# Optimization experiments

Measured on AMD Instinct MI355X. Metric: run time of the kernel, lower is better.

The kernel has to match this reference:

```python
import jax, jax.numpy as jnp
import numpy as np

B, N, E = 2, 20000, 160000
D, U = 1, 100          # input_dim, num_units
IN = D + U             # 101
NEG_SLOPE = 0.2        # PyG GATv2Conv default


def setup_inputs() -> dict:
    key = jax.random.key(0)
    ks = jax.random.split(key, 20)
    s = 0.1
    inp = {
        "inputs": jax.random.normal(ks[0], (B, N * D), jnp.float32),
        "state": jax.random.normal(ks[1], (B, N * U), jnp.float32),
        "src": jax.random.randint(ks[2], (E,), 0, N),
        "dst": jax.random.randint(ks[3], (E,), 0, N),
        # GATv2Conv(101, 200) params: lin_l, lin_r, att, out-bias
        "Wl1": jax.random.normal(ks[4], (IN, 2 * U), jnp.float32) * s,
        "bl1": jax.random.normal(ks[5], (2 * U,), jnp.float32) * s,
        "Wr1": jax.random.normal(ks[6], (IN, 2 * U), jnp.float32) * s,
        "br1": jax.random.normal(ks[7], (2 * U,), jnp.float32) * s,
        "att1": jax.random.normal(ks[8], (2 * U,), jnp.float32) * s,
        "bg1": jax.random.normal(ks[9], (2 * U,), jnp.float32) * s,
        "bias0": jax.random.normal(ks[10], (2 * U,), jnp.float32) * s,
        # GATv2Conv(101, 100) params
        "Wl2": jax.random.normal(ks[11], (IN, U), jnp.float32) * s,
        "bl2": jax.random.normal(ks[12], (U,), jnp.float32) * s,
        "Wr2": jax.random.normal(ks[13], (IN, U), jnp.float32) * s,
        "br2": jax.random.normal(ks[14], (U,), jnp.float32) * s,
        "att2": jax.random.normal(ks[15], (U,), jnp.float32) * s,
        "bg2": jax.random.normal(ks[16], (U,), jnp.float32) * s,
        "bias1": jax.random.normal(ks[17], (U,), jnp.float32) * s,
    }
    return inp


def _gatv2(x, src_f, dst_f, Wl, bl, Wr, br, att, bg):
    # x: (B, N, IN); edges (with self-loops) flow src -> dst.
    xl = x @ Wl + bl                                   # (B, N, C) source transform
    xr = x @ Wr + br                                   # (B, N, C) target transform
    msg = jax.nn.leaky_relu(xl[:, src_f] + xr[:, dst_f], NEG_SLOPE)  # (B, Ef, C)
    e = jnp.einsum('bec,c->be', msg, att)              # (B, Ef) attention logits
    seg_max = jax.vmap(lambda v: jax.ops.segment_max(v, dst_f, num_segments=N))(e)
    ea = jnp.exp(e - seg_max[:, dst_f])
    denom = jax.vmap(lambda v: jax.ops.segment_sum(v, dst_f, num_segments=N))(ea)
    alpha = ea / denom[:, dst_f]                       # per-target softmax
    out = jax.vmap(
        lambda a, xs: jax.ops.segment_sum(a[:, None] * xs, dst_f, num_segments=N)
    )(alpha, xl[:, src_f])                             # (B, N, C)
    return out + bg


def reference(inputs, state, src, dst,
              Wl1, bl1, Wr1, br1, att1, bg1, bias0,
              Wl2, bl2, Wr2, br2, att2, bg2, bias1):
    loops = jnp.arange(N)
    src_f = jnp.concatenate([src, loops])              # PyG adds self-loops
    dst_f = jnp.concatenate([dst, loops])
    inputs3 = inputs.reshape(B, N, D)
    state3 = state.reshape(B, N, U)

    # _gc1: GATv2(101 -> 200) + bias_0, sigmoid gates r, u
    xs = jnp.concatenate([inputs3, state3], axis=2)    # (B, N, 101)
    g1 = _gatv2(xs, src_f, dst_f, Wl1, bl1, Wr1, br1, att1, bg1) + bias0
    val = jax.nn.sigmoid(g1)                           # (B, N, 200)
    r = val[..., :U].reshape(B, N * U)
    u = val[..., U:].reshape(B, N * U)

    # _gc2: GATv2(101 -> 100) on [inputs, r*state] + bias_1, tanh
    xs2 = jnp.concatenate([inputs3, (r * state).reshape(B, N, U)], axis=2)
    c = jnp.tanh(_gatv2(xs2, src_f, dst_f, Wl2, bl2, Wr2, br2, att2, bg2) + bias1)
    c = c.reshape(B, N * U)

    new_state = u * state + (1.0 - u) * c              # (B, N*U)
    return new_state
```

## Files before the change

### kernel.cpp

```cpp
#include <hip/hip_runtime.h>
#include <stdint.h>

typedef __attribute__((ext_vector_type(8))) short short8;
typedef __attribute__((ext_vector_type(4))) short short4v;
typedef __attribute__((ext_vector_type(4))) float f32x4;

static constexpr int BB = 2, NN = 20000, UU = 100;
static constexpr int MT = BB * NN;
static constexpr int MPAD = 40192;
static constexpr float NEG = 0.2f;

__device__ __forceinline__ float b2f(short s) {
  union { uint32_t u; float f; } cv; cv.u = ((uint32_t)(uint16_t)s) << 16; return cv.f;
}
__device__ __forceinline__ short f2b(float x) {
  union { float f; uint32_t u; } cv; cv.f = x;
  uint32_t r = cv.u + 0x7FFFu + ((cv.u >> 16) & 1u);
  return (short)(r >> 16);
}

template<int CTRL>
__device__ __forceinline__ float dppadd(float x) {
  int v = __builtin_amdgcn_update_dpp(0, __float_as_int(x), CTRL, 0xF, 0xF, false);
  return x + __int_as_float(v);
}
__device__ __forceinline__ float red32(float x) {
  x = dppadd<0x121>(x);
  x = dppadd<0x122>(x);
  x = dppadd<0x124>(x);
  x = dppadd<0x128>(x);
  return x + __shfl_xor(x, 16);
}


__global__ void k_prep(const float* __restrict__ inp, const float* __restrict__ st,
                       const float* __restrict__ Wl1, const float* __restrict__ Wr1,
                       const float* __restrict__ Wl2, const float* __restrict__ Wr2,
                       short* __restrict__ A, short* __restrict__ BT1,
                       short* __restrict__ BT2, int* __restrict__ cursor) {
  int t = blockIdx.x * 256 + threadIdx.x;
  if (t < MT * 16) {
    int r = t >> 4, g = t & 15;
    short8 v;
#pragma unroll
    for (int j = 0; j < 8; ++j) {
      int e = g * 8 + j;
      float x = 0.f;
      if (e == 0) x = inp[r];
      else if (e <= 100) x = st[(size_t)r * 100 + e - 1];
      v[j] = f2b(x);
    }
    *(short8*)(A + (size_t)r * 128 + (g << 3)) = v;
  }
  if (t < 512 * 16) {
    int n = t >> 4, g = t & 15;
    short8 v;
#pragma unroll
    for (int j = 0; j < 8; ++j) {
      int k = g * 8 + j;
      float x = 0.f;
      if (k < 101 && n < 400)
        x = (n < 200) ? Wl1[(size_t)k * 200 + n] : Wr1[(size_t)k * 200 + n - 200];
      v[j] = f2b(x);
    }
    *(short8*)(BT1 + (size_t)n * 128 + (g << 3)) = v;
  }
  if (t < 256 * 16) {
    int n = t >> 4, g = t & 15;
    short8 v;
#pragma unroll
    for (int j = 0; j < 8; ++j) {
      int k = g * 8 + j;
      int ksrc = (k < 100) ? k + 1 : ((k == 100) ? 0 : -1);
      float x = 0.f;
      if (ksrc >= 0 && n < 200)
        x = (n < 100) ? Wl2[(size_t)ksrc * 100 + n] : Wr2[(size_t)ksrc * 100 + n - 100];
      v[j] = f2b(x);
    }
    *(short8*)(BT2 + (size_t)n * 128 + (g << 3)) = v;
  }
  if (t < NN) cursor[t] = 0;
}


__global__ void k_hist(const int* __restrict__ dst, int E, int* __restrict__ hist) {
  int e = blockIdx.x * 256 + threadIdx.x;
  if (e < E) atomicAdd(&hist[dst[e]], 1);
}

__global__ __launch_bounds__(1024) void k_scan(int* __restrict__ histcur,
                                               int* __restrict__ rowptr, int N, int E) {
  __shared__ int part[1024];
  int t = threadIdx.x;
  int CH = (N + 1023) / 1024;
  int beg = t * CH; if (beg > N) beg = N;
  int end = beg + CH; if (end > N) end = N;
  int s = 0;
  for (int i = beg; i < end; ++i) s += histcur[i];
  part[t] = s;
  __syncthreads();
  for (int off = 1; off < 1024; off <<= 1) {
    int v = (t >= off) ? part[t - off] : 0;
    __syncthreads();
    part[t] += v;
    __syncthreads();
  }
  int base = (t == 0) ? 0 : part[t - 1];
  for (int i = beg; i < end; ++i) {
    int h = histcur[i];
    rowptr[i] = base;
    histcur[i] = base;
    base += h;
  }
  if (t == 1023) rowptr[N] = part[1023];
}

__global__ void k_scatter(const int* __restrict__ src, const int* __restrict__ dst, int E,
                          int* __restrict__ cursor, int* __restrict__ col) {
  int e = blockIdx.x * 256 + threadIdx.x;
  if (e < E) {
    int p = atomicAdd(&cursor[dst[e]], 1);
    col[p] = src[e];
  }
}


template<int NOUT, int SPLIT>
__global__ __launch_bounds__(256) void k_gemmd(
    const short* __restrict__ A, const short* __restrict__ BT,
    const float* __restrict__ bias_l, const float* __restrict__ bias_r,
    short* __restrict__ X) {
  int w = threadIdx.x >> 6, lane = threadIdx.x & 63;
  int m0 = (blockIdx.x * 4 + w) * 64;
  int n0 = blockIdx.y * 64;
  int lrow = lane & 15, lk = lane >> 4;
  const short* Ab = A  + ((size_t)m0 + lrow) * 128 + lk * 8;
  const short* Bb = BT + ((size_t)n0 + lrow) * 128 + lk * 8;

  f32x4 acc[4][4];
#pragma unroll
  for (int i = 0; i < 4; ++i)
#pragma unroll
    for (int j = 0; j < 4; ++j) acc[i][j] = (f32x4){0.f, 0.f, 0.f, 0.f};

#pragma unroll
  for (int kk = 0; kk < 4; ++kk) {
    short8 a[4], b[4];
#pragma unroll
    for (int f = 0; f < 4; ++f) {
      a[f] = *(const short8*)(Ab + f * (16 * 128) + kk * 32);
      b[f] = *(const short8*)(Bb + f * (16 * 128) + kk * 32);
    }
#pragma unroll
    for (int i = 0; i < 4; ++i)
#pragma unroll
      for (int j = 0; j < 4; ++j)
        acc[i][j] = __builtin_amdgcn_mfma_f32_16x16x32_bf16(a[i], b[j], acc[i][j], 0, 0, 0);
  }

#pragma unroll
  for (int j = 0; j < 4; ++j) {
    int nc = n0 + j * 16 + lrow;
    bool nok = nc < NOUT;
    float bv = 0.f;
    int coff = 0;
    if (nok) {
      bv   = (nc < SPLIT) ? bias_l[nc] : bias_r[nc - SPLIT];
      coff = (nc < SPLIT) ? nc : 2 * SPLIT + (nc - SPLIT);
    }
#pragma unroll
    for (int i = 0; i < 4; ++i) {
      int mb = m0 + i * 16 + lk * 4;
#pragma unroll
      for (int r = 0; r < 4; ++r) {
        int m = mb + r;
        if (nok && m < MT) {
          int b_   = (m >= NN) ? 1 : 0;
          int node = m - b_ * NN;
          X[(size_t)node * (4 * SPLIT) + coff + b_ * SPLIT] = f2b(acc[i][j][r] + bv);
        }
      }
    }
  }
}


#define EDGE1(S, NUM, DEN, NCH, STRIDE)                                            \
  { short8 v_ = *(const short8*)(xb + (size_t)(S) * STRIDE);                       \
    float e_ = 0.f;                                                                \
    _Pragma("unroll") for (int q = 0; q < NCH; ++q) {                              \
      float x_ = b2f(v_[q]); float m_ = x_ + xrv[q];                               \
      m_ = (m_ > 0.f) ? m_ : NEG * m_; e_ = fmaf(m_, attv[q], e_); }               \
    e_ = red32(e_);                                                                \
    float p_ = __expf(e_); DEN += p_;                                              \
    _Pragma("unroll") for (int q = 0; q < NCH; ++q)                                \
      NUM[q] = fmaf(p_, b2f(v_[q]), NUM[q]); }

__global__ __launch_bounds__(256) void k_agg1(
    const short* __restrict__ X1, const int* __restrict__ rowptr, const int* __restrict__ col,
    const float* __restrict__ att, const float* __restrict__ bgv, const float* __restrict__ bias0,
    const float* __restrict__ st, const float* __restrict__ inp,
    short* __restrict__ A2, float* __restrict__ uu) {
  int w = threadIdx.x >> 6, lane = threadIdx.x & 63;
  int n = blockIdx.x * 4 + w;
  if (n >= NN) return;
  int half = lane >> 5, ll = lane & 31;
  int c0 = (ll < 25 ? ll : 24) * 8;
  int idx = half * NN + n;
  const short* xb = X1 + (size_t)half * 200 + c0;

  float attv[8], xrv[8], num[8];
  {
    f32x4 a0 = (f32x4){0,0,0,0}, a1 = (f32x4){0,0,0,0};
    if (ll < 25) { a0 = *(const f32x4*)(att + c0); a1 = *(const f32x4*)(att + c0 + 4); }
#pragma unroll
    for (int q = 0; q < 4; ++q) { attv[q] = a0[q]; attv[4 + q] = a1[q]; }
    short8 xr8 = *(const short8*)(X1 + (size_t)n * 800 + 400 + half * 200 + c0);
#pragma unroll
    for (int q = 0; q < 8; ++q) xrv[q] = (ll < 25) ? b2f(xr8[q]) : 0.f;
  }
  float denom;
  {
    short8 v = *(const short8*)(xb + (size_t)n * 800);
    float xs[8], e = 0.f;
#pragma unroll
    for (int q = 0; q < 8; ++q) {
      xs[q] = b2f(v[q]);
      float msg = xs[q] + xrv[q];
      msg = (msg > 0.f) ? msg : NEG * msg;
      e = fmaf(msg, attv[q], e);
    }
    e = red32(e);
    float pe = __expf(e);
    denom = pe;
#pragma unroll
    for (int q = 0; q < 8; ++q) num[q] = pe * xs[q];
  }

  int beg = rowptr[n], end = rowptr[n + 1];
  int deg = end - beg;
  int degc = min(deg, 64);
  int cv = 0;
  if (deg > 0) cv = col[beg + (lane < degc ? lane : 0)];
  int p = 0;
  for (; p + 2 <= degc; p += 2) {
    int s0 = __shfl(cv, p), s1 = __shfl(cv, p + 1);
    short8 v0 = *(const short8*)(xb + (size_t)s0 * 800);
    short8 v1 = *(const short8*)(xb + (size_t)s1 * 800);
    float e0 = 0.f, e1 = 0.f;
#pragma unroll
    for (int q = 0; q < 8; ++q) {
      float x, m_;
      x = b2f(v0[q]); m_ = x + xrv[q]; m_ = (m_ > 0.f) ? m_ : NEG * m_; e0 = fmaf(m_, attv[q], e0);
      x = b2f(v1[q]); m_ = x + xrv[q]; m_ = (m_ > 0.f) ? m_ : NEG * m_; e1 = fmaf(m_, attv[q], e1);
    }
    e0 = red32(e0); e1 = red32(e1);
    float pe0 = __expf(e0), pe1 = __expf(e1);
    denom += pe0 + pe1;
#pragma unroll
    for (int q = 0; q < 8; ++q)
      num[q] = fmaf(pe1, b2f(v1[q]), fmaf(pe0, b2f(v0[q]), num[q]));
  }
  if (p < degc) {
    int s0 = __shfl(cv, p);
    EDGE1(s0, num, denom, 8, 800);
  }
  for (int t = 64; t < deg; ++t) { int s = col[beg + t]; EDGE1(s, num, denom, 8, 800); }

  float invd = 1.f / denom;
  if (ll < 25) {
    f32x4 g0 = *(const f32x4*)(bgv + c0),   g1 = *(const f32x4*)(bgv + c0 + 4);
    f32x4 h0 = *(const f32x4*)(bias0 + c0), h1 = *(const f32x4*)(bias0 + c0 + 4);
    float vq[8];
#pragma unroll
    for (int q = 0; q < 4; ++q) {
      float o0 = fmaf(num[q], invd, g0[q] + h0[q]);
      vq[q] = 1.f / (1.f + __expf(-o0));
      float o1 = fmaf(num[4 + q], invd, g1[q] + h1[q]);
      vq[4 + q] = 1.f / (1.f + __expf(-o1));
    }
    size_t sb = (size_t)idx * UU;
    if (ll < 12) {
      f32x4 s0 = *(const f32x4*)(st + sb + c0), s1 = *(const f32x4*)(st + sb + c0 + 4);
      short8 wv;
#pragma unroll
      for (int q = 0; q < 4; ++q) { wv[q] = f2b(vq[q] * s0[q]); wv[4 + q] = f2b(vq[4 + q] * s1[q]); }
      *(short8*)(A2 + (size_t)idx * 128 + (ll << 3)) = wv;
    } else if (ll == 12) {
      f32x4 s0 = *(const f32x4*)(st + sb + 96);
      short8 wv;
#pragma unroll
      for (int q = 0; q < 4; ++q) wv[q] = f2b(vq[q] * s0[q]);
      wv[4] = f2b(inp[idx]); wv[5] = 0; wv[6] = 0; wv[7] = 0;
      *(short8*)(A2 + (size_t)idx * 128 + (12 << 3)) = wv;
      *(f32x4*)(uu + sb) = (f32x4){vq[4], vq[5], vq[6], vq[7]};
    } else {
      int uo = c0 - 100;
      *(f32x4*)(uu + sb + uo)     = (f32x4){vq[0], vq[1], vq[2], vq[3]};
      *(f32x4*)(uu + sb + uo + 4) = (f32x4){vq[4], vq[5], vq[6], vq[7]};
      if (ll < 16) {
        short8 z = (short8){0,0,0,0,0,0,0,0};
        *(short8*)(A2 + (size_t)idx * 128 + (ll << 3)) = z;
      }
    }
  }
}

__global__ __launch_bounds__(256) void k_agg2(
    const short* __restrict__ X2, const int* __restrict__ rowptr, const int* __restrict__ col,
    const float* __restrict__ att, const float* __restrict__ bgv, const float* __restrict__ bias1,
    const float* __restrict__ st, float* __restrict__ out) {
  int w = threadIdx.x >> 6, lane = threadIdx.x & 63;
  int n = blockIdx.x * 4 + w;
  if (n >= NN) return;
  int half = lane >> 5, ll = lane & 31;
  int c0 = (ll < 25 ? ll : 24) * 4;
  int idx = half * NN + n;
  const short* xb = X2 + (size_t)half * 100 + c0;

  float attv[4], xrv[4], num[4];
  {
    f32x4 a0 = (f32x4){0,0,0,0};
    if (ll < 25) a0 = *(const f32x4*)(att + c0);
#pragma unroll
    for (int q = 0; q < 4; ++q) attv[q] = a0[q];
    short4v xr4 = *(const short4v*)(X2 + (size_t)n * 400 + 200 + half * 100 + c0);
#pragma unroll
    for (int q = 0; q < 4; ++q) xrv[q] = (ll < 25) ? b2f(xr4[q]) : 0.f;
  }
  float denom;
  {
    short4v v = *(const short4v*)(xb + (size_t)n * 400);
    float xs[4], e = 0.f;
#pragma unroll
    for (int q = 0; q < 4; ++q) {
      xs[q] = b2f(v[q]);
      float msg = xs[q] + xrv[q];
      msg = (msg > 0.f) ? msg : NEG * msg;
      e = fmaf(msg, attv[q], e);
    }
    e = red32(e);
    float pe = __expf(e);
    denom = pe;
#pragma unroll
    for (int q = 0; q < 4; ++q) num[q] = pe * xs[q];
  }

  int beg = rowptr[n], end = rowptr[n + 1];
  int deg = end - beg;
  int degc = min(deg, 64);
  int cv = 0;
  if (deg > 0) cv = col[beg + (lane < degc ? lane : 0)];
  int p = 0;
  for (; p + 2 <= degc; p += 2) {
    int s0 = __shfl(cv, p), s1 = __shfl(cv, p + 1);
    short4v v0 = *(const short4v*)(xb + (size_t)s0 * 400);
    short4v v1 = *(const short4v*)(xb + (size_t)s1 * 400);
    float e0 = 0.f, e1 = 0.f;
#pragma unroll
    for (int q = 0; q < 4; ++q) {
      float x, m_;
      x = b2f(v0[q]); m_ = x + xrv[q]; m_ = (m_ > 0.f) ? m_ : NEG * m_; e0 = fmaf(m_, attv[q], e0);
      x = b2f(v1[q]); m_ = x + xrv[q]; m_ = (m_ > 0.f) ? m_ : NEG * m_; e1 = fmaf(m_, attv[q], e1);
    }
    e0 = red32(e0); e1 = red32(e1);
    float pe0 = __expf(e0), pe1 = __expf(e1);
    denom += pe0 + pe1;
#pragma unroll
    for (int q = 0; q < 4; ++q)
      num[q] = fmaf(pe1, b2f(v1[q]), fmaf(pe0, b2f(v0[q]), num[q]));
  }
  if (p < degc) {
    int s0 = __shfl(cv, p);
    { short4v v_ = *(const short4v*)(xb + (size_t)s0 * 400);
      float e_ = 0.f;
#pragma unroll
      for (int q = 0; q < 4; ++q) {
        float x_ = b2f(v_[q]); float m_ = x_ + xrv[q];
        m_ = (m_ > 0.f) ? m_ : NEG * m_; e_ = fmaf(m_, attv[q], e_);
      }
      e_ = red32(e_);
      float p_ = __expf(e_); denom += p_;
#pragma unroll
      for (int q = 0; q < 4; ++q) num[q] = fmaf(p_, b2f(v_[q]), num[q]);
    }
  }
  for (int t = 64; t < deg; ++t) {
    int s = col[beg + t];
    { short4v v_ = *(const short4v*)(xb + (size_t)s * 400);
      float e_ = 0.f;
#pragma unroll
      for (int q = 0; q < 4; ++q) {
        float x_ = b2f(v_[q]); float m_ = x_ + xrv[q];
        m_ = (m_ > 0.f) ? m_ : NEG * m_; e_ = fmaf(m_, attv[q], e_);
      }
      e_ = red32(e_);
      float p_ = __expf(e_); denom += p_;
#pragma unroll
      for (int q = 0; q < 4; ++q) num[q] = fmaf(p_, b2f(v_[q]), num[q]);
    }
  }

  float invd = 1.f / denom;
  if (ll < 25) {
    f32x4 g0 = *(const f32x4*)(bgv + c0);
    f32x4 h0 = *(const f32x4*)(bias1 + c0);
    size_t sb = (size_t)idx * UU;
    f32x4 uv = *(const f32x4*)(out + sb + c0);
    f32x4 sv = *(const f32x4*)(st + sb + c0);
    f32x4 res;
#pragma unroll
    for (int q = 0; q < 4; ++q) {
      float o   = fmaf(num[q], invd, g0[q] + h0[q]);
      float cvh = tanhf(o);
      res[q] = uv[q] * sv[q] + (1.f - uv[q]) * cvh;
    }
    *(f32x4*)(out + sb + c0) = res;
  }
}


extern "C" void kernel_launch(void* const* d_in, const int* in_sizes, int n_in,
                              void* d_out, int out_size, void* d_ws, size_t ws_size,
                              hipStream_t stream) {
  const float* inp  = (const float*)d_in[0];
  const float* st   = (const float*)d_in[1];
  const int*   src  = (const int*)d_in[2];
  const int*   dst  = (const int*)d_in[3];
  const float* Wl1  = (const float*)d_in[4];
  const float* bl1  = (const float*)d_in[5];
  const float* Wr1  = (const float*)d_in[6];
  const float* br1  = (const float*)d_in[7];
  const float* att1 = (const float*)d_in[8];
  const float* bg1  = (const float*)d_in[9];
  const float* bias0= (const float*)d_in[10];
  const float* Wl2  = (const float*)d_in[11];
  const float* bl2  = (const float*)d_in[12];
  const float* Wr2  = (const float*)d_in[13];
  const float* br2  = (const float*)d_in[14];
  const float* att2 = (const float*)d_in[15];
  const float* bg2  = (const float*)d_in[16];
  const float* bias1= (const float*)d_in[17];

  const int N = NN;
  const int E = in_sizes[2];

  short* X1  = (short*)d_ws;
  short* X2  = X1;
  short* Aws = X1 + (size_t)NN * 800;
  short* BT1 = Aws + (size_t)MPAD * 128;
  short* BT2 = BT1 + 512 * 128;
  int* rowptr = (int*)(BT2 + 256 * 128);
  int* cursor = rowptr + (N + 1);
  int* col    = cursor + N;

  k_prep<<<(MT * 16 + 255) / 256, 256, 0, stream>>>(inp, st, Wl1, Wr1, Wl2, Wr2,
                                                    Aws, BT1, BT2, cursor);
  k_hist<<<(E + 255) / 256, 256, 0, stream>>>(dst, E, cursor);
  k_scan<<<1, 1024, 0, stream>>>(cursor, rowptr, N, E);
  k_scatter<<<(E + 255) / 256, 256, 0, stream>>>(src, dst, E, cursor, col);
  {
    dim3 g(157, 8);
    k_gemmd<400, 200><<<g, 256, 0, stream>>>(Aws, BT1, bl1, br1, X1);
  }
  k_agg1<<<(NN + 3) / 4, 256, 0, stream>>>(X1, rowptr, col, att1, bg1, bias0, st, inp,
                                           Aws, (float*)d_out);
  {
    dim3 g(157, 4);
    k_gemmd<200, 100><<<g, 256, 0, stream>>>(Aws, BT2, bl2, br2, X2);
  }
  k_agg2<<<(NN + 3) / 4, 256, 0, stream>>>(X2, rowptr, col, att2, bg2, bias1, st,
                                           (float*)d_out);
}
```

Measured before the change: 192.8 us.

## Keep A tile in registers across two N tiles and vectorize GEMM output stores

Each GEMM wavefront now loads its 64-row A fragment once into registers and reuses it across two 64-column output tiles, which halves the grid's y dimension and cuts repeated A reads. The MFMA operands are swapped so each lane holds four consecutive output channels, letting the epilogue load the bias as a float4 and write four bf16 values in one 8-byte store instead of scalar scattered writes. This raises register pressure (16 short8 A fragments held live) and halves the number of blocks, which lowers occupancy and parallelism.

```diff
diff --git a/kernel.cpp b/kernel.cpp
--- a/kernel.cpp
+++ b/kernel.cpp
@@ -125,59 +125,62 @@
 }
 
 
-template<int NOUT, int SPLIT>
+template<int NOUT, int SPLIT, int NTW>
 __global__ __launch_bounds__(256) void k_gemmd(
     const short* __restrict__ A, const short* __restrict__ BT,
     const float* __restrict__ bias_l, const float* __restrict__ bias_r,
     short* __restrict__ X) {
   int w = threadIdx.x >> 6, lane = threadIdx.x & 63;
   int m0 = (blockIdx.x * 4 + w) * 64;
-  int n0 = blockIdx.y * 64;
   int lrow = lane & 15, lk = lane >> 4;
-  const short* Ab = A  + ((size_t)m0 + lrow) * 128 + lk * 8;
-  const short* Bb = BT + ((size_t)n0 + lrow) * 128 + lk * 8;
-
-  f32x4 acc[4][4];
-#pragma unroll
-  for (int i = 0; i < 4; ++i)
-#pragma unroll
-    for (int j = 0; j < 4; ++j) acc[i][j] = (f32x4){0.f, 0.f, 0.f, 0.f};
-
-#pragma unroll
-  for (int kk = 0; kk < 4; ++kk) {
-    short8 a[4], b[4];
-#pragma unroll
-    for (int f = 0; f < 4; ++f) {
-      a[f] = *(const short8*)(Ab + f * (16 * 128) + kk * 32);
-      b[f] = *(const short8*)(Bb + f * (16 * 128) + kk * 32);
-    }
+
+  short8 a[4][4];
+#pragma unroll
+  for (int kk = 0; kk < 4; ++kk)
+#pragma unroll
+    for (int j = 0; j < 4; ++j)
+      a[kk][j] = *(const short8*)(A + ((size_t)m0 + j * 16 + lrow) * 128 + lk * 8 + kk * 32);
+
+#pragma unroll
+  for (int nt = 0; nt < NTW; ++nt) {
+    int nbase = (blockIdx.y * NTW + nt) * 64;
+    f32x4 acc[4][4];
 #pragma unroll
     for (int i = 0; i < 4; ++i)
 #pragma unroll
-      for (int j = 0; j < 4; ++j)
-        acc[i][j] = __builtin_amdgcn_mfma_f32_16x16x32_bf16(a[i], b[j], acc[i][j], 0, 0, 0);
-  }
-
-#pragma unroll
-  for (int j = 0; j < 4; ++j) {
-    int nc = n0 + j * 16 + lrow;
-    bool nok = nc < NOUT;
-    float bv = 0.f;
-    int coff = 0;
-    if (nok) {
-      bv   = (nc < SPLIT) ? bias_l[nc] : bias_r[nc - SPLIT];
-      coff = (nc < SPLIT) ? nc : 2 * SPLIT + (nc - SPLIT);
-    }
+      for (int j = 0; j < 4; ++j) acc[i][j] = (f32x4){0.f, 0.f, 0.f, 0.f};
+
+#pragma unroll
+    for (int kk = 0; kk < 4; ++kk) {
+      short8 b[4];
+#pragma unroll
+      for (int i = 0; i < 4; ++i)
+        b[i] = *(const short8*)(BT + ((size_t)nbase + i * 16 + lrow) * 128 + lk * 8 + kk * 32);
+#pragma unroll
+      for (int i = 0; i < 4; ++i)
+#pragma unroll
+        for (int j = 0; j < 4; ++j)
+          acc[i][j] = __builtin_amdgcn_mfma_f32_16x16x32_bf16(b[i], a[kk][j], acc[i][j], 0, 0, 0);
+    }
+
 #pragma unroll
     for (int i = 0; i < 4; ++i) {
-      int mb = m0 + i * 16 + lk * 4;
-#pragma unroll
-      for (int r = 0; r < 4; ++r) {
-        int m = mb + r;
-        if (nok && m < MT) {
-          int b_   = (m >= NN) ? 1 : 0;
-          int node = m - b_ * NN;
-          X[(size_t)node * (4 * SPLIT) + coff + b_ * SPLIT] = f2b(acc[i][j][r] + bv);
+      int ch = nbase + i * 16 + lk * 4;
+      if (ch < NOUT) {
+        f32x4 bv = (ch < SPLIT) ? *(const f32x4*)(bias_l + ch)
+                                : *(const f32x4*)(bias_r + (ch - SPLIT));
+        int cbase = (ch < SPLIT) ? ch : 2 * SPLIT + (ch - SPLIT);
+#pragma unroll
+        for (int j = 0; j < 4; ++j) {
+          int m = m0 + j * 16 + lrow;
+          if (m < MT) {
+            int b_   = (m >= NN) ? 1 : 0;
+            int node = m - b_ * NN;
+            short4v wv;
+#pragma unroll
+            for (int r = 0; r < 4; ++r) wv[r] = f2b(acc[i][j][r] + bv[r]);
+            *(short4v*)(X + (size_t)node * (4 * SPLIT) + cbase + b_ * SPLIT) = wv;
+          }
         }
       }
     }
@@ -460,14 +463,14 @@
   k_scan<<<1, 1024, 0, stream>>>(cursor, rowptr, N, E);
   k_scatter<<<(E + 255) / 256, 256, 0, stream>>>(src, dst, E, cursor, col);
   {
-    dim3 g(157, 8);
-    k_gemmd<400, 200><<<g, 256, 0, stream>>>(Aws, BT1, bl1, br1, X1);
+    dim3 g(157, 4);
+    k_gemmd<400, 200, 2><<<g, 256, 0, stream>>>(Aws, BT1, bl1, br1, X1);
   }
   k_agg1<<<(NN + 3) / 4, 256, 0, stream>>>(X1, rowptr, col, att1, bg1, bias0, st, inp,
                                            Aws, (float*)d_out);
   {
-    dim3 g(157, 4);
-    k_gemmd<200, 100><<<g, 256, 0, stream>>>(Aws, BT2, bl2, br2, X2);
+    dim3 g(157, 2);
+    k_gemmd<200, 100, 2><<<g, 256, 0, stream>>>(Aws, BT2, bl2, br2, X2);
   }
   k_agg2<<<(NN + 3) / 4, 256, 0, stream>>>(X2, rowptr, col, att2, bg2, bias1, st,
                                            (float*)d_out);
```

Result: faster. 178.9 us (-7.2%).
